# Kernel tuning notes

Measured on AMD Instinct MI355X. Metric: run time of the kernel, lower is better.

The kernel has to match this reference:

```python
import jax, jax.numpy as jnp
import numpy as np

D_MODEL = 4096
D_STATE = 16
DT_RANK = D_MODEL // 16  # 'auto'
BATCH = 1024


def setup_inputs() -> dict:
    key = jax.random.key(0)
    ks = jax.random.split(key, 8)
    x = jax.random.normal(ks[0], (BATCH, D_MODEL), dtype=jnp.float32)
    h = jax.random.normal(ks[1], (BATCH, D_MODEL, D_STATE), dtype=jnp.float32)
    # x_proj: Linear(d_model -> dt_rank + 2*d_state), no bias
    W_xproj = jax.random.normal(ks[2], (DT_RANK + 2 * D_STATE, D_MODEL), dtype=jnp.float32) * 0.02
    # dt_proj: Linear(dt_rank -> d_model), bias initialized to inv-softplus of dt
    dt_init_std = DT_RANK ** (-0.5)
    W_dt = jax.random.uniform(ks[3], (D_MODEL, DT_RANK), dtype=jnp.float32,
                              minval=-dt_init_std, maxval=dt_init_std)
    dt = jnp.exp(jax.random.uniform(ks[4], (D_MODEL,), dtype=jnp.float32)
                 * (np.log(0.1) - np.log(0.001)) + np.log(0.001))
    b_dt = dt + jnp.log(-jnp.expm1(-dt))  # inverse softplus
    A_log = jnp.log(jnp.arange(1, D_STATE + 1, dtype=jnp.float32))
    D = jnp.ones((D_MODEL,), dtype=jnp.float32)
    W_out = jax.random.normal(ks[5], (D_MODEL, D_MODEL), dtype=jnp.float32) * 0.02
    return {"x": x, "h": h, "W_xproj": W_xproj, "W_dt": W_dt, "b_dt": b_dt,
            "A_log": A_log, "D": D, "W_out": W_out}


def reference(x, h, W_xproj, W_dt, b_dt, A_log, D, W_out):
    # x: (b, d)  h: (b, d, n)
    xp = x @ W_xproj.T                      # (b, dt_rank + 2n)
    delta_raw = xp[:, :DT_RANK]
    B = xp[:, DT_RANK:DT_RANK + D_STATE]    # (b, n)
    C = xp[:, DT_RANK + D_STATE:]           # (b, n)
    delta = jax.nn.softplus(delta_raw @ W_dt.T + b_dt)  # (b, d)
    A = -jnp.exp(A_log)                     # (n,)
    A_bar = jnp.exp(delta[:, :, None] * A[None, None, :])    # (b, d, n)
    B_bar = delta[:, :, None] * B[:, None, :]                 # (b, d, n)
    h_new = A_bar * h + B_bar * x[:, :, None]                 # (b, d, n)
    y = jnp.einsum('bn,bdn->bd', C, h_new)
    y = y + D * x
    y = y @ W_out.T
    return y, h_new
```

## Files before the change

### kernel.cpp

```cpp
#include <hip/hip_runtime.h>
#include <stdint.h>

#define BATCH  1024
#define DMODEL 4096
#define DSTATE 16
#define DTRANK 256
#define NPROJ  288

typedef short  short8 __attribute__((ext_vector_type(8)));
typedef __bf16 bf16x8 __attribute__((ext_vector_type(8)));
typedef float  f32x4  __attribute__((ext_vector_type(4)));

static __device__ __forceinline__ short f2bf(float f) {
  uint32_t u = __float_as_uint(f);
  u = (u + 0x7fffu + ((u >> 16) & 1u)) >> 16;
  return (short)u;
}
static __device__ __forceinline__ float bf2f(short s) {
  return __uint_as_float(((uint32_t)(uint16_t)s) << 16);
}

static __device__ __forceinline__ void gl_lds16(const void* g, void* lds) {
  __builtin_amdgcn_global_load_lds(
      (const __attribute__((address_space(1))) void*)g,
      (__attribute__((address_space(3))) void*)lds, 16, 0, 0);
}

template<bool LO>
__global__ __launch_bounds__(256) void cvt_hilo(const float* __restrict__ in,
                                                short* __restrict__ outH,
                                                short* __restrict__ outL, int n8) {
  const int i = blockIdx.x * 256 + threadIdx.x;
  if (i >= n8) return;
  const float4* p = (const float4*)in + (size_t)i * 2;
  float4 v0 = p[0], v1 = p[1];
  float vv[8] = {v0.x, v0.y, v0.z, v0.w, v1.x, v1.y, v1.z, v1.w};
  short hh[8], ll[8];
  #pragma unroll
  for (int j = 0; j < 8; ++j) {
    hh[j] = f2bf(vv[j]);
    ll[j] = f2bf(vv[j] - bf2f(hh[j]));
  }
  ((short8*)outH)[i] = *(const short8*)hh;
  if (LO) ((short8*)outL)[i] = *(const short8*)ll;
}

__global__ __launch_bounds__(256) void cvt_xp(const float* __restrict__ xp,
                                              short* __restrict__ outH,
                                              short* __restrict__ outL) {
  const int i = blockIdx.x * 256 + threadIdx.x;
  const int b = i >> 5, c = (i & 31) << 3;
  const float* p = xp + (size_t)b * NPROJ + c;
  float4 v0 = *(const float4*)p, v1 = *(const float4*)(p + 4);
  float vv[8] = {v0.x, v0.y, v0.z, v0.w, v1.x, v1.y, v1.z, v1.w};
  short hh[8], ll[8];
  #pragma unroll
  for (int j = 0; j < 8; ++j) {
    hh[j] = f2bf(vv[j]);
    ll[j] = f2bf(vv[j] - bf2f(hh[j]));
  }
  ((short8*)outH)[i] = *(const short8*)hh;
  ((short8*)outL)[i] = *(const short8*)ll;
}

template<bool SPLIT, bool ATOMIC, bool SOFTPLUS>
__global__ __launch_bounds__(256) void gemm_lds(
    const short* __restrict__ AH, const short* __restrict__ AL, int lda,
    const short* __restrict__ BH, const short* __restrict__ BL, int ldb, int nB,
    float* __restrict__ C, int ldc,
    const float* __restrict__ bias, int k_len)
{
  const int bn = blockIdx.x, bm = blockIdx.y;
  const int kbase0 = blockIdx.z * k_len;
  const int tid = threadIdx.x;
  const int lane = tid & 63, wave = tid >> 6;
  const int wm = (wave & 1) << 6, wn = (wave >> 1) << 6;
  const int row = lane & 15, quad = lane >> 4;

  __shared__ short AsH[4096], BsH[4096], AsL[4096], BsL[4096];

  f32x4 acc[4][4];
  #pragma unroll
  for (int i = 0; i < 4; ++i)
    #pragma unroll
    for (int j = 0; j < 4; ++j) acc[i][j] = (f32x4){0.f, 0.f, 0.f, 0.f};

  const int c0 = (wave << 7) + lane, c1 = c0 + 64;
  const int m0 = c0 & 127, k0 = c0 >> 7;
  const int m1 = c1 & 127, k1 = c1 >> 7;
  const size_t arow0 = (size_t)((bm << 7) + m0) * lda + (k0 << 3);
  const size_t arow1 = (size_t)((bm << 7) + m1) * lda + (k1 << 3);
  const size_t brow0 = (size_t)((bn << 7) + m0) * ldb + (k0 << 3);
  const size_t brow1 = (size_t)((bn << 7) + m1) * ldb + (k1 << 3);
  short* lA0 = &AsH[c0 << 3]; short* lA1 = &AsH[c1 << 3];
  short* lB0 = &BsH[c0 << 3]; short* lB1 = &BsH[c1 << 3];
  short* lAL0 = &AsL[c0 << 3]; short* lAL1 = &AsL[c1 << 3];
  short* lBL0 = &BsL[c0 << 3]; short* lBL1 = &BsL[c1 << 3];

  const int nsteps = k_len >> 5;
  for (int ks = 0; ks < nsteps; ++ks) {
    const int kb = kbase0 + (ks << 5);
    __syncthreads();
    gl_lds16(AH + arow0 + kb, lA0);
    gl_lds16(AH + arow1 + kb, lA1);
    gl_lds16(BH + brow0 + kb, lB0);
    gl_lds16(BH + brow1 + kb, lB1);
    if (SPLIT) {
      gl_lds16(AL + arow0 + kb, lAL0);
      gl_lds16(AL + arow1 + kb, lAL1);
      gl_lds16(BL + brow0 + kb, lBL0);
      gl_lds16(BL + brow1 + kb, lBL1);
    }
    __syncthreads();

    short8 aH[4], bH[4], aL[4], bL[4];
    #pragma unroll
    for (int i = 0; i < 4; ++i) {
      const int ao = (((quad << 7) + wm + (i << 4) + row) << 3);
      const int bo = (((quad << 7) + wn + (i << 4) + row) << 3);
      aH[i] = *(short8*)&AsH[ao];
      bH[i] = *(short8*)&BsH[bo];
      if (SPLIT) {
        aL[i] = *(short8*)&AsL[ao];
        bL[i] = *(short8*)&BsL[bo];
      }
    }
    #pragma unroll
    for (int mi = 0; mi < 4; ++mi)
      #pragma unroll
      for (int ni = 0; ni < 4; ++ni) {
        acc[mi][ni] = __builtin_amdgcn_mfma_f32_16x16x32_bf16(
            __builtin_bit_cast(bf16x8, aH[mi]), __builtin_bit_cast(bf16x8, bH[ni]),
            acc[mi][ni], 0, 0, 0);
        if (SPLIT) {
          acc[mi][ni] = __builtin_amdgcn_mfma_f32_16x16x32_bf16(
              __builtin_bit_cast(bf16x8, aH[mi]), __builtin_bit_cast(bf16x8, bL[ni]),
              acc[mi][ni], 0, 0, 0);
          acc[mi][ni] = __builtin_amdgcn_mfma_f32_16x16x32_bf16(
              __builtin_bit_cast(bf16x8, aL[mi]), __builtin_bit_cast(bf16x8, bH[ni]),
              acc[mi][ni], 0, 0, 0);
        }
      }
  }

  #pragma unroll
  for (int mi = 0; mi < 4; ++mi) {
    #pragma unroll
    for (int ni = 0; ni < 4; ++ni) {
      const int rbase = (bm << 7) + wm + (mi << 4) + (quad << 2);
      const int cg = (bn << 7) + wn + (ni << 4) + row;
      if (cg < nB) {
        #pragma unroll
        for (int r = 0; r < 4; ++r) {
          float v = acc[mi][ni][r];
          if (SOFTPLUS) {
            float t = v + bias[cg];
            v = fmaxf(t, 0.f) + log1pf(__expf(-fabsf(t)));
          }
          if (ATOMIC) atomicAdd(&C[(size_t)(rbase + r) * ldc + cg], v);
          else        C[(size_t)(rbase + r) * ldc + cg] = v;
        }
      }
    }
  }
}

__global__ __launch_bounds__(256) void ssm_update(
    const float* __restrict__ x, const float* __restrict__ h,
    const float* __restrict__ xp, const float* __restrict__ delta,
    const float* __restrict__ A_log, const float* __restrict__ Dv,
    float* __restrict__ out, short* __restrict__ ypre)
{
  const int b = blockIdx.y;
  const int d = (blockIdx.x << 8) + threadIdx.x;
  __shared__ float Bs[DSTATE], Cs[DSTATE], Aa[DSTATE];
  if (threadIdx.x < DSTATE) {
    const int t = threadIdx.x;
    Bs[t] = xp[b * NPROJ + DTRANK + t];
    Cs[t] = xp[b * NPROJ + DTRANK + DSTATE + t];
    Aa[t] = -__expf(A_log[t]);
  }
  __syncthreads();
  const size_t bd = (size_t)b * DMODEL + d;
  const float dl = delta[bd];
  const float xv = x[bd];
  const float4* hp = (const float4*)(h + bd * 16);
  float4* ho = (float4*)(out + (size_t)BATCH * DMODEL + bd * 16);
  float y = 0.f;
  #pragma unroll
  for (int g = 0; g < 4; ++g) {
    float4 hv = hp[g];
    float4 o;
    o.x = __expf(dl * Aa[4*g+0]) * hv.x + dl * Bs[4*g+0] * xv; y = fmaf(Cs[4*g+0], o.x, y);
    o.y = __expf(dl * Aa[4*g+1]) * hv.y + dl * Bs[4*g+1] * xv; y = fmaf(Cs[4*g+1], o.y, y);
    o.z = __expf(dl * Aa[4*g+2]) * hv.z + dl * Bs[4*g+2] * xv; y = fmaf(Cs[4*g+2], o.z, y);
    o.w = __expf(dl * Aa[4*g+3]) * hv.w + dl * Bs[4*g+3] * xv; y = fmaf(Cs[4*g+3], o.w, y);
    ho[g] = o;
  }
  y = fmaf(Dv[d], xv, y);
  ypre[bd] = f2bf(y);
}

extern "C" void kernel_launch(void* const* d_in, const int* in_sizes, int n_in,
                              void* d_out, int out_size, void* d_ws, size_t ws_size,
                              hipStream_t stream)
{
  const float* x    = (const float*)d_in[0];
  const float* h    = (const float*)d_in[1];
  const float* Wx   = (const float*)d_in[2];
  const float* Wdt  = (const float*)d_in[3];
  const float* bdt  = (const float*)d_in[4];
  const float* Alog = (const float*)d_in[5];
  const float* Dv   = (const float*)d_in[6];
  const float* Wout = (const float*)d_in[7];
  float* out = (float*)d_out;

  char* ws = (char*)d_ws;
  size_t off = 0;
  auto alloc = [&](size_t bytes) { char* p = ws + off; off += (bytes + 255) & ~(size_t)255; return p; };
  float* xp    = (float*)alloc((size_t)BATCH * NPROJ * 4);
  float* delta = (float*)alloc((size_t)BATCH * DMODEL * 4);
  short* ypre  = (short*)alloc((size_t)BATCH * DMODEL * 2);
  short* xH    = (short*)alloc((size_t)BATCH * DMODEL * 2);
  short* xL    = (short*)alloc((size_t)BATCH * DMODEL * 2);
  short* WxH   = (short*)alloc((size_t)384 * DMODEL * 2);
  short* WxL   = (short*)alloc((size_t)384 * DMODEL * 2);
  short* WdtH  = (short*)alloc((size_t)DMODEL * DTRANK * 2);
  short* WdtL  = (short*)alloc((size_t)DMODEL * DTRANK * 2);
  short* xpH   = (short*)alloc((size_t)BATCH * DTRANK * 2);
  short* xpL   = (short*)alloc((size_t)BATCH * DTRANK * 2);
  short* WoutH = (short*)alloc((size_t)DMODEL * DMODEL * 2);

  cvt_hilo<true><<<dim3((BATCH * DMODEL / 8 + 255) / 256), 256, 0, stream>>>(x, xH, xL, BATCH * DMODEL / 8);
  cvt_hilo<true><<<dim3((NPROJ * DMODEL / 8 + 255) / 256), 256, 0, stream>>>(Wx, WxH, WxL, NPROJ * DMODEL / 8);
  cvt_hilo<true><<<dim3((DMODEL * DTRANK / 8 + 255) / 256), 256, 0, stream>>>(Wdt, WdtH, WdtL, DMODEL * DTRANK / 8);
  cvt_hilo<false><<<dim3((DMODEL * DMODEL / 8 + 255) / 256), 256, 0, stream>>>(Wout, WoutH, nullptr, DMODEL * DMODEL / 8);
  hipMemsetAsync(xp, 0, (size_t)BATCH * NPROJ * 4, stream);

  gemm_lds<true, true, false><<<dim3(3, 8, 8), 256, 0, stream>>>(
      xH, xL, DMODEL, WxH, WxL, DMODEL, NPROJ, xp, NPROJ, nullptr, 512);
  cvt_xp<<<dim3(BATCH * DTRANK / 8 / 256), 256, 0, stream>>>(xp, xpH, xpL);
  gemm_lds<true, false, true><<<dim3(32, 8, 1), 256, 0, stream>>>(
      xpH, xpL, DTRANK, WdtH, WdtL, DTRANK, DMODEL, delta, DMODEL, bdt, DTRANK);
  ssm_update<<<dim3(16, BATCH), 256, 0, stream>>>(x, h, xp, delta, Alog, Dv, out, ypre);
  gemm_lds<false, false, false><<<dim3(32, 8, 1), 256, 0, stream>>>(
      ypre, nullptr, DMODEL, WoutH, nullptr, DMODEL, DMODEL, out, DMODEL, nullptr, DMODEL);
}
```

Baseline: 766.8 us.

## Use split-K with partial buffers and reduce kernels across all three GEMMs

Replaces the atomic-add split-K in the x_proj GEMM with per-split partial buffers plus a vectorized reduce kernel, and raises its split factor. It also splits the dt_proj GEMM in two and the output GEMM in four, so more blocks run on the many CUs. The softplus and bias for delta move into ssm_update, which sums the two partials. This trades extra workspace memory and extra global read/write traffic for more parallelism and no atomics or memset.

```diff
diff --git a/kernel.cpp b/kernel.cpp
--- a/kernel.cpp
+++ b/kernel.cpp
@@ -63,21 +63,37 @@
   ((short8*)outL)[i] = *(const short8*)ll;
 }
 
-template<bool SPLIT, bool ATOMIC, bool SOFTPLUS>
+template<int N>
+__global__ __launch_bounds__(256) void reduce_add(const float* __restrict__ in,
+                                                  size_t stride,
+                                                  float* __restrict__ out, int n4) {
+  const int i = blockIdx.x * 256 + threadIdx.x;
+  if (i >= n4) return;
+  float4 s = ((const float4*)in)[i];
+  #pragma unroll
+  for (int j = 1; j < N; ++j) {
+    float4 v = ((const float4*)(in + (size_t)j * stride))[i];
+    s.x += v.x; s.y += v.y; s.z += v.z; s.w += v.w;
+  }
+  ((float4*)out)[i] = s;
+}
+
+template<bool SPLIT>
 __global__ __launch_bounds__(256) void gemm_lds(
     const short* __restrict__ AH, const short* __restrict__ AL, int lda,
     const short* __restrict__ BH, const short* __restrict__ BL, int ldb, int nB,
-    float* __restrict__ C, int ldc,
-    const float* __restrict__ bias, int k_len)
+    float* __restrict__ C, int ldc, size_t cz_stride, int k_len)
 {
   const int bn = blockIdx.x, bm = blockIdx.y;
   const int kbase0 = blockIdx.z * k_len;
+  float* __restrict__ Cz = C + (size_t)blockIdx.z * cz_stride;
   const int tid = threadIdx.x;
   const int lane = tid & 63, wave = tid >> 6;
   const int wm = (wave & 1) << 6, wn = (wave >> 1) << 6;
   const int row = lane & 15, quad = lane >> 4;
 
-  __shared__ short AsH[4096], BsH[4096], AsL[4096], BsL[4096];
+  __shared__ short AsH[4096], BsH[4096];
+  __shared__ short AsL[SPLIT ? 4096 : 4], BsL[SPLIT ? 4096 : 4];
 
   f32x4 acc[4][4];
   #pragma unroll
@@ -94,8 +110,12 @@
   const size_t brow1 = (size_t)((bn << 7) + m1) * ldb + (k1 << 3);
   short* lA0 = &AsH[c0 << 3]; short* lA1 = &AsH[c1 << 3];
   short* lB0 = &BsH[c0 << 3]; short* lB1 = &BsH[c1 << 3];
-  short* lAL0 = &AsL[c0 << 3]; short* lAL1 = &AsL[c1 << 3];
-  short* lBL0 = &BsL[c0 << 3]; short* lBL1 = &BsL[c1 << 3];
+  short* lAL0 = nullptr; short* lAL1 = nullptr;
+  short* lBL0 = nullptr; short* lBL1 = nullptr;
+  if constexpr (SPLIT) {
+    lAL0 = &AsL[c0 << 3]; lAL1 = &AsL[c1 << 3];
+    lBL0 = &BsL[c0 << 3]; lBL1 = &BsL[c1 << 3];
+  }
 
   const int nsteps = k_len >> 5;
   for (int ks = 0; ks < nsteps; ++ks) {
@@ -105,7 +125,7 @@
     gl_lds16(AH + arow1 + kb, lA1);
     gl_lds16(BH + brow0 + kb, lB0);
     gl_lds16(BH + brow1 + kb, lB1);
-    if (SPLIT) {
+    if constexpr (SPLIT) {
       gl_lds16(AL + arow0 + kb, lAL0);
       gl_lds16(AL + arow1 + kb, lAL1);
       gl_lds16(BL + brow0 + kb, lBL0);
@@ -120,7 +140,7 @@
       const int bo = (((quad << 7) + wn + (i << 4) + row) << 3);
       aH[i] = *(short8*)&AsH[ao];
       bH[i] = *(short8*)&BsH[bo];
-      if (SPLIT) {
+      if constexpr (SPLIT) {
         aL[i] = *(short8*)&AsL[ao];
         bL[i] = *(short8*)&BsL[bo];
       }
@@ -132,7 +152,7 @@
         acc[mi][ni] = __builtin_amdgcn_mfma_f32_16x16x32_bf16(
             __builtin_bit_cast(bf16x8, aH[mi]), __builtin_bit_cast(bf16x8, bH[ni]),
             acc[mi][ni], 0, 0, 0);
-        if (SPLIT) {
+        if constexpr (SPLIT) {
           acc[mi][ni] = __builtin_amdgcn_mfma_f32_16x16x32_bf16(
               __builtin_bit_cast(bf16x8, aH[mi]), __builtin_bit_cast(bf16x8, bL[ni]),
               acc[mi][ni], 0, 0, 0);
@@ -152,13 +172,7 @@
       if (cg < nB) {
         #pragma unroll
         for (int r = 0; r < 4; ++r) {
-          float v = acc[mi][ni][r];
-          if (SOFTPLUS) {
-            float t = v + bias[cg];
-            v = fmaxf(t, 0.f) + log1pf(__expf(-fabsf(t)));
-          }
-          if (ATOMIC) atomicAdd(&C[(size_t)(rbase + r) * ldc + cg], v);
-          else        C[(size_t)(rbase + r) * ldc + cg] = v;
+          Cz[(size_t)(rbase + r) * ldc + cg] = acc[mi][ni][r];
         }
       }
     }
@@ -167,7 +181,8 @@
 
 __global__ __launch_bounds__(256) void ssm_update(
     const float* __restrict__ x, const float* __restrict__ h,
-    const float* __restrict__ xp, const float* __restrict__ delta,
+    const float* __restrict__ xp, const float* __restrict__ dP,
+    const float* __restrict__ bdt,
     const float* __restrict__ A_log, const float* __restrict__ Dv,
     float* __restrict__ out, short* __restrict__ ypre)
 {
@@ -182,7 +197,8 @@
   }
   __syncthreads();
   const size_t bd = (size_t)b * DMODEL + d;
-  const float dl = delta[bd];
+  const float traw = dP[bd] + dP[bd + (size_t)BATCH * DMODEL] + bdt[d];
+  const float dl = fmaxf(traw, 0.f) + log1pf(__expf(-fabsf(traw)));
   const float xv = x[bd];
   const float4* hp = (const float4*)(h + bd * 16);
   float4* ho = (float4*)(out + (size_t)BATCH * DMODEL + bd * 16);
@@ -219,7 +235,9 @@
   size_t off = 0;
   auto alloc = [&](size_t bytes) { char* p = ws + off; off += (bytes + 255) & ~(size_t)255; return p; };
   float* xp    = (float*)alloc((size_t)BATCH * NPROJ * 4);
-  float* delta = (float*)alloc((size_t)BATCH * DMODEL * 4);
+  float* xpP   = (float*)alloc((size_t)16 * BATCH * NPROJ * 4);
+  float* dP    = (float*)alloc((size_t)2 * BATCH * DMODEL * 4);
+  float* yP    = (float*)alloc((size_t)4 * BATCH * DMODEL * 4);
   short* ypre  = (short*)alloc((size_t)BATCH * DMODEL * 2);
   short* xH    = (short*)alloc((size_t)BATCH * DMODEL * 2);
   short* xL    = (short*)alloc((size_t)BATCH * DMODEL * 2);
@@ -235,14 +253,21 @@
   cvt_hilo<true><<<dim3((NPROJ * DMODEL / 8 + 255) / 256), 256, 0, stream>>>(Wx, WxH, WxL, NPROJ * DMODEL / 8);
   cvt_hilo<true><<<dim3((DMODEL * DTRANK / 8 + 255) / 256), 256, 0, stream>>>(Wdt, WdtH, WdtL, DMODEL * DTRANK / 8);
   cvt_hilo<false><<<dim3((DMODEL * DMODEL / 8 + 255) / 256), 256, 0, stream>>>(Wout, WoutH, nullptr, DMODEL * DMODEL / 8);
-  hipMemsetAsync(xp, 0, (size_t)BATCH * NPROJ * 4, stream);
-
-  gemm_lds<true, true, false><<<dim3(3, 8, 8), 256, 0, stream>>>(
-      xH, xL, DMODEL, WxH, WxL, DMODEL, NPROJ, xp, NPROJ, nullptr, 512);
+
+  gemm_lds<true><<<dim3(3, 8, 16), 256, 0, stream>>>(
+      xH, xL, DMODEL, WxH, WxL, DMODEL, NPROJ, xpP, NPROJ, (size_t)BATCH * NPROJ, 256);
+  reduce_add<16><<<dim3(BATCH * NPROJ / 4 / 256), 256, 0, stream>>>(
+      xpP, (size_t)BATCH * NPROJ, xp, BATCH * NPROJ / 4);
+
   cvt_xp<<<dim3(BATCH * DTRANK / 8 / 256), 256, 0, stream>>>(xp, xpH, xpL);
-  gemm_lds<true, false, true><<<dim3(32, 8, 1), 256, 0, stream>>>(
-      xpH, xpL, DTRANK, WdtH, WdtL, DTRANK, DMODEL, delta, DMODEL, bdt, DTRANK);
-  ssm_update<<<dim3(16, BATCH), 256, 0, stream>>>(x, h, xp, delta, Alog, Dv, out, ypre);
-  gemm_lds<false, false, false><<<dim3(32, 8, 1), 256, 0, stream>>>(
-      ypre, nullptr, DMODEL, WoutH, nullptr, DMODEL, DMODEL, out, DMODEL, nullptr, DMODEL);
-}
+
+  gemm_lds<true><<<dim3(32, 8, 2), 256, 0, stream>>>(
+      xpH, xpL, DTRANK, WdtH, WdtL, DTRANK, DMODEL, dP, DMODEL, (size_t)BATCH * DMODEL, 128);
+
+  ssm_update<<<dim3(16, BATCH), 256, 0, stream>>>(x, h, xp, dP, bdt, Alog, Dv, out, ypre);
+
+  gemm_lds<false><<<dim3(32, 8, 4), 256, 0, stream>>>(
+      ypre, nullptr, DMODEL, WoutH, nullptr, DMODEL, DMODEL, yP, DMODEL, (size_t)BATCH * DMODEL, 1024);
+  reduce_add<4><<<dim3(BATCH * DMODEL / 4 / 256), 256, 0, stream>>>(
+      yP, (size_t)BATCH * DMODEL, out, BATCH * DMODEL / 4);
+}
```

Result: faster. 698.9 us (-8.9%).
